# Kernel optimization log

Hardware: AMD Instinct MI355X
Metric: run time of the kernel (lower is better)

## Reference

```python
import jax, jax.numpy as jnp
import numpy as np

N_NODES = 60
N_EDGES = 1800
BATCH = 8192
NEG_SLOPE = 0.2  # PyG GATConv default leaky_relu slope


def _conv2d(x, w, b):
    y = jax.lax.conv_general_dilated(x, w, window_strides=(1, 1), padding='VALID',
                                     dimension_numbers=('NCHW', 'OIHW', 'NCHW'))
    return y + b[None, :, None, None]


def _maxpool2(x):
    return jax.lax.reduce_window(x, -jnp.inf, jax.lax.max, (1, 1, 2, 2), (1, 1, 2, 2), 'VALID')


def _gat(x, src, dst, edge_attr, W, a_src, a_dst, We, a_edge, b, n):
    # PyG GATConv, heads=1: xl = x W ; alpha_e = leakyrelu(a_src.xl[src] + a_dst.xl[dst] + a_edge.(edge_attr We))
    xl = x @ W                                    # [N, out]
    asrc = (xl * a_src).sum(-1)                   # [N]
    adst = (xl * a_dst).sum(-1)                   # [N]
    aedge = ((edge_attr @ We) * a_edge).sum(-1)   # [E]
    alpha = jax.nn.leaky_relu(asrc[src] + adst[dst] + aedge, NEG_SLOPE)
    # softmax over incoming edges of each dst node
    m = jax.ops.segment_max(alpha, dst, num_segments=n)
    ex = jnp.exp(alpha - m[dst])
    denom = jax.ops.segment_sum(ex, dst, num_segments=n)
    w_e = ex / denom[dst]
    out = jax.ops.segment_sum(w_e[:, None] * xl[src], dst, num_segments=n)
    return out + b


def _batchnorm_gnn(x):
    # torch code uses .item(): mean/std are detached python floats
    avg = jax.lax.stop_gradient(x.mean())
    std = jax.lax.stop_gradient(jnp.sqrt(((x - avg) ** 2).mean()))
    return (x - avg) / std


def setup_inputs() -> dict:
    key = jax.random.key(0)
    ks = jax.random.split(key, 24)
    f = lambda k, shape, scale=0.1: (jax.random.normal(k, shape, dtype=jnp.float32) * scale)
    inp = {
        'node_fea': jax.random.normal(ks[0], (N_NODES, 1), dtype=jnp.float32),
        'edge_fea': jax.random.normal(ks[1], (N_EDGES, 1), dtype=jnp.float32),
        'pic_fea': jax.random.normal(ks[2], (BATCH, 3, 32, 32), dtype=jnp.float32),
        'conv1_w': f(ks[3], (6, 3, 5, 5)), 'conv1_b': f(ks[4], (6,)),
        'conv2_w': f(ks[5], (16, 6, 5, 5)), 'conv2_b': f(ks[6], (16,)),
        'gat1_w': f(ks[7], (1, 6), 0.5), 'gat1_att_src': f(ks[8], (6,), 0.5),
        'gat1_att_dst': f(ks[9], (6,), 0.5), 'gat1_lin_edge': f(ks[10], (1, 6), 0.5),
        'gat1_att_edge': f(ks[11], (6,), 0.5), 'gat1_b': f(ks[12], (6,)),
        'gat2_w': f(ks[13], (6, 16), 0.3), 'gat2_att_src': f(ks[14], (16,), 0.3),
        'gat2_att_dst': f(ks[15], (16,), 0.3), 'gat2_lin_edge': f(ks[16], (1, 16), 0.3),
        'gat2_att_edge': f(ks[17], (16,), 0.3), 'gat2_b': f(ks[18], (16,)),
        'fc1_w': f(ks[19], (1360, 512), 0.03), 'fc1_b': f(ks[20], (512,)),
        'fc2_w': f(ks[21], (512, 10), 0.05), 'fc2_b': f(ks[22], (10,)),
        'edge_index': jax.random.randint(ks[23], (2, N_EDGES), 0, N_NODES, dtype=jnp.int64 if jax.config.jax_enable_x64 else jnp.int32),
    }
    return inp


def reference(node_fea, edge_fea, pic_fea,
              conv1_w, conv1_b, conv2_w, conv2_b,
              gat1_w, gat1_att_src, gat1_att_dst, gat1_lin_edge, gat1_att_edge, gat1_b,
              gat2_w, gat2_att_src, gat2_att_dst, gat2_lin_edge, gat2_att_edge, gat2_b,
              fc1_w, fc1_b, fc2_w, fc2_b, edge_index):
    n = node_fea.shape[0]
    # CNN branch: 32 -> 28 -> 14 -> 10 -> 5
    p = _maxpool2(jax.nn.relu(_conv2d(pic_fea, conv1_w, conv1_b)))
    p = _maxpool2(jax.nn.relu(_conv2d(p, conv2_w, conv2_b)))
    p = p.reshape(p.shape[0], -1)  # [B, 400]
    # add self loops (PyG default, fill_value='mean' for edge_attr)
    loop = jnp.arange(n)
    src = jnp.concatenate([edge_index[0], loop])
    dst = jnp.concatenate([edge_index[1], loop])
    ea = jnp.concatenate([edge_fea, jnp.broadcast_to(edge_fea.mean(0, keepdims=True), (n, edge_fea.shape[1]))], axis=0)
    # GNN branch
    x = _gat(node_fea, src, dst, ea, gat1_w, gat1_att_src, gat1_att_dst, gat1_lin_edge, gat1_att_edge, gat1_b, n)
    x = jax.nn.relu(_batchnorm_gnn(x))
    x = _gat(x, src, dst, ea, gat2_w, gat2_att_src, gat2_att_dst, gat2_lin_edge, gat2_att_edge, gat2_b, n)
    x = jax.nn.relu(_batchnorm_gnn(x))
    g = x.reshape(-1)  # [960]
    feat = jnp.concatenate([jnp.broadcast_to(g, (p.shape[0], g.shape[0])), p], axis=1)  # [B, 1360]
    h = jax.nn.relu(feat @ fc1_w + fc1_b)
    return jnp.tanh(h @ fc2_w + fc2_b)
```

## Files before the change

kernel.cpp:

```cpp
#include <hip/hip_runtime.h>
#include <math.h>

#define N_NODES 60
#define N_EDGES 1800
#define N_ETOT  1860
#define SLOPE   0.2f

#define SROW 36
#define SCH  (32 * SROW)
#define CROW 15
#define CCH  (14 * CROW)

struct ConvS {
    float simg[3 * SCH];
    float sw1[450];
    float sb1[8];
    float sw2[2400];
    float sb2[16];
    float c1[6 * CCH];
};
struct GnnS {
    float ea[N_ETOT];
    float alpha[N_ETOT];
    float x_in[960];
    float xl[960];
    float outb[960];
    float as_[N_NODES], ad_[N_NODES], den_[N_NODES];
    float red[256];
    unsigned char srcs[N_ETOT], dsts[N_ETOT];
    unsigned short csr[N_ETOT];
    int cnt[N_NODES], off[N_NODES + 4];
};
union SMem { ConvS c; GnnS g; };

__device__ __forceinline__ void block_reduce_sum(float v, float* red, float* out) {
    int tid = threadIdx.x;
    red[tid] = v;
    __syncthreads();
    for (int st = 128; st > 0; st >>= 1) {
        if (tid < st) red[tid] += red[tid + st];
        __syncthreads();
    }
    *out = red[0];
    __syncthreads();
}

__device__ void gat_layer(GnnS& S, const float* x_in, int in_dim, int out_dim,
                          const float* W, const float* a_src, const float* a_dst,
                          const float* We, const float* a_edge, const float* bias,
                          float* xl, float* outb) {
    const int tid = threadIdx.x, nt = blockDim.x;
    for (int idx = tid; idx < N_NODES * out_dim; idx += nt) {
        int i = idx / out_dim, j = idx % out_dim;
        float s = 0.f;
        for (int k = 0; k < in_dim; ++k) s += x_in[i * in_dim + k] * W[k * out_dim + j];
        xl[idx] = s;
    }
    __syncthreads();
    for (int i = tid; i < N_NODES; i += nt) {
        float s = 0.f, d = 0.f;
        for (int j = 0; j < out_dim; ++j) {
            s += xl[i * out_dim + j] * a_src[j];
            d += xl[i * out_dim + j] * a_dst[j];
        }
        S.as_[i] = s; S.ad_[i] = d;
    }
    float ecoef = 0.f;
    for (int j = 0; j < out_dim; ++j) ecoef += We[j] * a_edge[j];
    __syncthreads();
    for (int e = tid; e < N_ETOT; e += nt) {
        float a = S.as_[S.srcs[e]] + S.ad_[S.dsts[e]] + S.ea[e] * ecoef;
        S.alpha[e] = (a >= 0.f) ? a : SLOPE * a;
    }
    __syncthreads();
    for (int d = tid; d < N_NODES; d += nt) {
        float m = -INFINITY;
        for (int k = S.off[d]; k < S.off[d + 1]; ++k) m = fmaxf(m, S.alpha[S.csr[k]]);
        float den = 0.f;
        for (int k = S.off[d]; k < S.off[d + 1]; ++k) {
            int e = S.csr[k];
            float ex = expf(S.alpha[e] - m);
            S.alpha[e] = ex;
            den += ex;
        }
        S.den_[d] = den;
    }
    __syncthreads();
    for (int idx = tid; idx < N_NODES * out_dim; idx += nt) {
        int d = idx / out_dim, j = idx % out_dim;
        float s = 0.f;
        for (int k = S.off[d]; k < S.off[d + 1]; ++k) {
            int e = S.csr[k];
            s += S.alpha[e] * xl[(int)S.srcs[e] * out_dim + j];
        }
        outb[idx] = s / S.den_[d] + bias[j];
    }
    __syncthreads();
}

__device__ void bn_relu(GnnS& S, const float* v, float* dst, int n) {
    const int tid = threadIdx.x, nt = blockDim.x;
    float s = 0.f;
    for (int i = tid; i < n; i += nt) s += v[i];
    float tot;
    block_reduce_sum(s, S.red, &tot);
    float avg = tot / n;
    float s2 = 0.f;
    for (int i = tid; i < n; i += nt) { float d = v[i] - avg; s2 += d * d; }
    block_reduce_sum(s2, S.red, &tot);
    float stdv = sqrtf(tot / n);
    for (int i = tid; i < n; i += nt) dst[i] = fmaxf((v[i] - avg) / stdv, 0.f);
    __syncthreads();
}

__device__ void gnn_path(GnnS& S,
    const float* node_fea, const float* edge_fea, const int* eidx,
    const float* g1w, const float* g1as, const float* g1ad,
    const float* g1we, const float* g1ae, const float* g1b,
    const float* g2w, const float* g2as, const float* g2ad,
    const float* g2we, const float* g2ae, const float* g2b,
    const float* fc1w, const float* fc1b, float* gcontrib) {
    const int tid = threadIdx.x, nt = blockDim.x;
    float s = 0.f;
    for (int e = tid; e < N_EDGES; e += nt) s += edge_fea[e];
    float tot;
    block_reduce_sum(s, S.red, &tot);
    float emean = tot / N_EDGES;
    for (int e = tid; e < N_ETOT; e += nt) {
        if (e < N_EDGES) {
            S.ea[e] = edge_fea[e];
            S.srcs[e] = (unsigned char)eidx[e];
            S.dsts[e] = (unsigned char)eidx[N_EDGES + e];
        } else {
            S.ea[e] = emean;
            S.srcs[e] = (unsigned char)(e - N_EDGES);
            S.dsts[e] = (unsigned char)(e - N_EDGES);
        }
    }
    if (tid < N_NODES) S.x_in[tid] = node_fea[tid];
    __syncthreads();
    if (tid < N_NODES) {
        int c = 0;
        for (int e = 0; e < N_ETOT; ++e) c += (S.dsts[e] == tid);
        S.cnt[tid] = c;
    }
    __syncthreads();
    if (tid == 0) {
        S.off[0] = 0;
        for (int d = 0; d < N_NODES; ++d) S.off[d + 1] = S.off[d] + S.cnt[d];
    }
    __syncthreads();
    if (tid < N_NODES) {
        int k = S.off[tid];
        for (int e = 0; e < N_ETOT; ++e)
            if (S.dsts[e] == tid) S.csr[k++] = (unsigned short)e;
    }
    __syncthreads();

    gat_layer(S, S.x_in, 1, 6, g1w, g1as, g1ad, g1we, g1ae, g1b, S.xl, S.outb);
    bn_relu(S, S.outb, S.x_in, N_NODES * 6);
    gat_layer(S, S.x_in, 6, 16, g2w, g2as, g2ad, g2we, g2ae, g2b, S.xl, S.outb);
    bn_relu(S, S.outb, S.x_in, N_NODES * 16);

    for (int j = tid; j < 512; j += nt) {
        float acc = fc1b[j];
#pragma unroll 4
        for (int k = 0; k < 960; ++k) acc += S.x_in[k] * fc1w[(size_t)k * 512 + j];
        gcontrib[j] = acc;
    }
}

__device__ void conv_path(ConvS& C, int b,
                          const float* __restrict__ pic,
                          const float* __restrict__ w1, const float* __restrict__ b1,
                          const float* __restrict__ w2, const float* __restrict__ b2,
                          float* __restrict__ p) {
    const int tid = threadIdx.x;
    const float* img = pic + (size_t)b * 3072;
    for (int i = tid; i < 3072; i += 256) {
        int ic = i >> 10, rem = i & 1023, y = rem >> 5, x = rem & 31;
        C.simg[ic * SCH + y * SROW + x] = img[i];
    }
    for (int i = tid; i < 450; i += 256) C.sw1[i] = w1[i];
    if (tid < 6) C.sb1[tid] = b1[tid];
    for (int i = tid; i < 2400; i += 256) C.sw2[i] = w2[i];
    if (tid < 16) C.sb2[tid] = b2[tid];
    __syncthreads();

    for (int it = tid; it < 588; it += 256) {
        int oc = it / 98, r = it % 98, py = r / 7, q = r % 7;
        int y0 = 2 * py, x0 = 4 * q;
        float bias = C.sb1[oc];
        float acc[2][4];
#pragma unroll
        for (int dy = 0; dy < 2; ++dy)
#pragma unroll
            for (int xi = 0; xi < 4; ++xi) acc[dy][xi] = bias;
        for (int ic = 0; ic < 3; ++ic) {
            float wr[25];
            const float* wp = &C.sw1[oc * 75 + ic * 25];
#pragma unroll
            for (int t = 0; t < 25; ++t) wr[t] = wp[t];
            const int base = ic * SCH + y0 * SROW + x0;
#pragma unroll
            for (int i = 0; i < 6; ++i) {
                const float4* rp = (const float4*)&C.simg[base + i * SROW];
                float4 va = rp[0], vb = rp[1];
                float row[8] = {va.x, va.y, va.z, va.w, vb.x, vb.y, vb.z, vb.w};
#pragma unroll
                for (int dy = 0; dy < 2; ++dy) {
                    int ky = i - dy;
                    if (ky >= 0 && ky < 5) {
#pragma unroll
                        for (int xi = 0; xi < 4; ++xi) {
                            float s = 0.f;
#pragma unroll
                            for (int kx = 0; kx < 5; ++kx)
                                s += row[xi + kx] * wr[ky * 5 + kx];
                            acc[dy][xi] += s;
                        }
                    }
                }
            }
        }
#pragma unroll
        for (int sx = 0; sx < 2; ++sx) {
            float mx = fmaxf(fmaxf(acc[0][2 * sx], acc[0][2 * sx + 1]),
                             fmaxf(acc[1][2 * sx], acc[1][2 * sx + 1]));
            C.c1[oc * CCH + py * CROW + 2 * q + sx] = fmaxf(mx, 0.f);
        }
    }
    __syncthreads();

    if (tid < 240) {
        int oc = tid / 15, r = tid % 15, py = r / 3, g = r % 3;
        int y0 = 2 * py, x0 = 4 * g;
        float bias = C.sb2[oc];
        float acc[2][4];
#pragma unroll
        for (int dy = 0; dy < 2; ++dy)
#pragma unroll
            for (int xi = 0; xi < 4; ++xi) acc[dy][xi] = bias;
        for (int ic = 0; ic < 6; ++ic) {
            float wr[25];
            const float* wp = &C.sw2[oc * 150 + ic * 25];
#pragma unroll
            for (int t = 0; t < 25; ++t) wr[t] = wp[t];
            const int base = ic * CCH + y0 * CROW + x0;
#pragma unroll
            for (int i = 0; i < 6; ++i) {
                float row[8];
#pragma unroll
                for (int j = 0; j < 8; ++j) row[j] = C.c1[base + i * CROW + j];
#pragma unroll
                for (int dy = 0; dy < 2; ++dy) {
                    int ky = i - dy;
                    if (ky >= 0 && ky < 5) {
#pragma unroll
                        for (int xi = 0; xi < 4; ++xi) {
                            float s = 0.f;
#pragma unroll
                            for (int kx = 0; kx < 5; ++kx)
                                s += row[xi + kx] * wr[ky * 5 + kx];
                            acc[dy][xi] += s;
                        }
                    }
                }
            }
        }
        int nsx = (g < 2) ? 2 : 1;
        for (int sx = 0; sx < nsx; ++sx) {
            float mx = fmaxf(fmaxf(acc[0][2 * sx], acc[0][2 * sx + 1]),
                             fmaxf(acc[1][2 * sx], acc[1][2 * sx + 1]));
            p[(size_t)b * 400 + oc * 25 + py * 5 + 2 * g + sx] = fmaxf(mx, 0.f);
        }
    }
}

__global__ void __launch_bounds__(256, 4) fused_kernel(
    const float* __restrict__ node_fea, const float* __restrict__ edge_fea,
    const int* __restrict__ eidx,
    const float* g1w, const float* g1as, const float* g1ad,
    const float* g1we, const float* g1ae, const float* g1b,
    const float* g2w, const float* g2as, const float* g2ad,
    const float* g2we, const float* g2ae, const float* g2b,
    const float* __restrict__ fc1w, const float* __restrict__ fc1b,
    float* __restrict__ gcontrib,
    const float* __restrict__ pic,
    const float* __restrict__ c1w, const float* __restrict__ c1b,
    const float* __restrict__ c2w, const float* __restrict__ c2b,
    float* __restrict__ p) {
    __shared__ SMem u;
    if (blockIdx.x == 0) {
        gnn_path(u.g, node_fea, edge_fea, eidx,
                 g1w, g1as, g1ad, g1we, g1ae, g1b,
                 g2w, g2as, g2ad, g2we, g2ae, g2b,
                 fc1w, fc1b, gcontrib);
    } else {
        conv_path(u.c, blockIdx.x - 1, pic, c1w, c1b, c2w, c2b, p);
    }
}

#define FC1_ROWS 16
__global__ void __launch_bounds__(256) fc1_kernel(
    const float* __restrict__ p, const float* __restrict__ w,
    const float* __restrict__ gcontrib, float* __restrict__ h) {
    __shared__ float sp[FC1_ROWS * 400];
    const int tid = threadIdx.x;
    const size_t r0 = (size_t)blockIdx.x * FC1_ROWS;
    for (int i = tid; i < FC1_ROWS * 400; i += 256) sp[i] = p[r0 * 400 + i];
    __syncthreads();
    const int c0 = tid, c1 = tid + 256;
    float acc[FC1_ROWS][2];
#pragma unroll
    for (int r = 0; r < FC1_ROWS; ++r) { acc[r][0] = 0.f; acc[r][1] = 0.f; }
    for (int k = 0; k < 400; k += 4) {
        float wa0 = w[(size_t)(k + 0) * 512 + c0], wa1 = w[(size_t)(k + 0) * 512 + c1];
        float wb0 = w[(size_t)(k + 1) * 512 + c0], wb1 = w[(size_t)(k + 1) * 512 + c1];
        float wc0 = w[(size_t)(k + 2) * 512 + c0], wc1 = w[(size_t)(k + 2) * 512 + c1];
        float wd0 = w[(size_t)(k + 3) * 512 + c0], wd1 = w[(size_t)(k + 3) * 512 + c1];
#pragma unroll
        for (int r = 0; r < FC1_ROWS; ++r) {
            float4 pv = *(const float4*)&sp[r * 400 + k];
            acc[r][0] += pv.x * wa0 + pv.y * wb0 + pv.z * wc0 + pv.w * wd0;
            acc[r][1] += pv.x * wa1 + pv.y * wb1 + pv.z * wc1 + pv.w * wd1;
        }
    }
    float g0 = gcontrib[c0], g1 = gcontrib[c1];
#pragma unroll
    for (int r = 0; r < FC1_ROWS; ++r) {
        h[(r0 + r) * 512 + c0] = fmaxf(acc[r][0] + g0, 0.f);
        h[(r0 + r) * 512 + c1] = fmaxf(acc[r][1] + g1, 0.f);
    }
}

__global__ void __launch_bounds__(256) fc2_kernel(
    const float* __restrict__ h, const float* __restrict__ w,
    const float* __restrict__ b, float* __restrict__ out) {
    const int wave = threadIdx.x >> 6, lane = threadIdx.x & 63;
    const size_t row = (size_t)blockIdx.x * 4 + wave;
    const float* hr = h + row * 512;
    float partial[10];
#pragma unroll
    for (int j = 0; j < 10; ++j) partial[j] = 0.f;
    for (int k = lane; k < 512; k += 64) {
        float hv = hr[k];
        const float* wr = w + (size_t)k * 10;
#pragma unroll
        for (int j = 0; j < 10; ++j) partial[j] += hv * wr[j];
    }
#pragma unroll
    for (int j = 0; j < 10; ++j) {
        float v = partial[j];
        for (int sft = 32; sft > 0; sft >>= 1) v += __shfl_xor(v, sft, 64);
        partial[j] = v;
    }
    if (lane == 0) {
#pragma unroll
        for (int j = 0; j < 10; ++j)
            out[row * 10 + j] = tanhf(partial[j] + b[j]);
    }
}

extern "C" void kernel_launch(void* const* d_in, const int* in_sizes, int n_in,
                              void* d_out, int out_size, void* d_ws, size_t ws_size,
                              hipStream_t stream) {
    const float* node_fea = (const float*)d_in[0];
    const float* edge_fea = (const float*)d_in[1];
    const float* pic      = (const float*)d_in[2];
    const float* c1w = (const float*)d_in[3];
    const float* c1b = (const float*)d_in[4];
    const float* c2w = (const float*)d_in[5];
    const float* c2b = (const float*)d_in[6];
    const float* g1w  = (const float*)d_in[7];
    const float* g1as = (const float*)d_in[8];
    const float* g1ad = (const float*)d_in[9];
    const float* g1we = (const float*)d_in[10];
    const float* g1ae = (const float*)d_in[11];
    const float* g1b  = (const float*)d_in[12];
    const float* g2w  = (const float*)d_in[13];
    const float* g2as = (const float*)d_in[14];
    const float* g2ad = (const float*)d_in[15];
    const float* g2we = (const float*)d_in[16];
    const float* g2ae = (const float*)d_in[17];
    const float* g2b  = (const float*)d_in[18];
    const float* fc1w = (const float*)d_in[19];
    const float* fc1b = (const float*)d_in[20];
    const float* fc2w = (const float*)d_in[21];
    const float* fc2b = (const float*)d_in[22];
    const int*   eidx = (const int*)d_in[23];
    float* out = (float*)d_out;

    char* ws = (char*)d_ws;
    float* gcontrib = (float*)ws;
    float* p = (float*)(ws + 2048);
    float* h = (float*)(ws + 2048 + (size_t)8192 * 400 * 4);

    hipLaunchKernelGGL(fused_kernel, dim3(8193), dim3(256), 0, stream,
                       node_fea, edge_fea, eidx,
                       g1w, g1as, g1ad, g1we, g1ae, g1b,
                       g2w, g2as, g2ad, g2we, g2ae, g2b,
                       fc1w, fc1b, gcontrib,
                       pic, c1w, c1b, c2w, c2b, p);
    hipLaunchKernelGGL(fc1_kernel, dim3(8192 / FC1_ROWS), dim3(256), 0, stream,
                       p, fc1w + (size_t)960 * 512, gcontrib, h);
    hipLaunchKernelGGL(fc2_kernel, dim3(8192 / 4), dim3(256), 0, stream,
                       h, fc2w, fc2b, out);
}
```

Measured before the change: 490.7 us.

## Retune conv shared-memory layout, thread mapping and occupancy; slim GNN smem

```diff
diff --git a/kernel.cpp b/kernel.cpp
--- a/kernel.cpp
+++ b/kernel.cpp
@@ -6,25 +6,21 @@
 #define N_ETOT  1860
 #define SLOPE   0.2f
 
-#define SROW 36
+#define SROW 34
 #define SCH  (32 * SROW)
-#define CROW 15
+#define CROW 16
 #define CCH  (14 * CROW)
-
 struct ConvS {
     float simg[3 * SCH];
-    float sw1[450];
-    float sb1[8];
-    float sw2[2400];
-    float sb2[16];
+    float sw1[456], sb1[8];
+    float sw2[2400], sb2[16];
     float c1[6 * CCH];
+    float pad[8];
 };
 struct GnnS {
-    float ea[N_ETOT];
     float alpha[N_ETOT];
     float x_in[960];
     float xl[960];
-    float outb[960];
     float as_[N_NODES], ad_[N_NODES], den_[N_NODES];
     float red[256];
     unsigned char srcs[N_ETOT], dsts[N_ETOT];
@@ -48,6 +44,7 @@
 __device__ void gat_layer(GnnS& S, const float* x_in, int in_dim, int out_dim,
                           const float* W, const float* a_src, const float* a_dst,
                           const float* We, const float* a_edge, const float* bias,
+                          const float* edge_fea, float emean,
                           float* xl, float* outb) {
     const int tid = threadIdx.x, nt = blockDim.x;
     for (int idx = tid; idx < N_NODES * out_dim; idx += nt) {
@@ -69,7 +66,8 @@
     for (int j = 0; j < out_dim; ++j) ecoef += We[j] * a_edge[j];
     __syncthreads();
     for (int e = tid; e < N_ETOT; e += nt) {
-        float a = S.as_[S.srcs[e]] + S.ad_[S.dsts[e]] + S.ea[e] * ecoef;
+        float eaval = (e < N_EDGES) ? edge_fea[e] : emean;
+        float a = S.as_[S.srcs[e]] + S.ad_[S.dsts[e]] + eaval * ecoef;
         S.alpha[e] = (a >= 0.f) ? a : SLOPE * a;
     }
     __syncthreads();
@@ -98,7 +96,7 @@
     __syncthreads();
 }
 
-__device__ void bn_relu(GnnS& S, const float* v, float* dst, int n) {
+__device__ void bn_relu(GnnS& S, float* v, int n) {
     const int tid = threadIdx.x, nt = blockDim.x;
     float s = 0.f;
     for (int i = tid; i < n; i += nt) s += v[i];
@@ -109,7 +107,8 @@
     for (int i = tid; i < n; i += nt) { float d = v[i] - avg; s2 += d * d; }
     block_reduce_sum(s2, S.red, &tot);
     float stdv = sqrtf(tot / n);
-    for (int i = tid; i < n; i += nt) dst[i] = fmaxf((v[i] - avg) / stdv, 0.f);
+    __syncthreads();
+    for (int i = tid; i < n; i += nt) v[i] = fmaxf((v[i] - avg) / stdv, 0.f);
     __syncthreads();
 }
 
@@ -128,11 +127,9 @@
     float emean = tot / N_EDGES;
     for (int e = tid; e < N_ETOT; e += nt) {
         if (e < N_EDGES) {
-            S.ea[e] = edge_fea[e];
             S.srcs[e] = (unsigned char)eidx[e];
             S.dsts[e] = (unsigned char)eidx[N_EDGES + e];
         } else {
-            S.ea[e] = emean;
             S.srcs[e] = (unsigned char)(e - N_EDGES);
             S.dsts[e] = (unsigned char)(e - N_EDGES);
         }
@@ -157,10 +154,12 @@
     }
     __syncthreads();
 
-    gat_layer(S, S.x_in, 1, 6, g1w, g1as, g1ad, g1we, g1ae, g1b, S.xl, S.outb);
-    bn_relu(S, S.outb, S.x_in, N_NODES * 6);
-    gat_layer(S, S.x_in, 6, 16, g2w, g2as, g2ad, g2we, g2ae, g2b, S.xl, S.outb);
-    bn_relu(S, S.outb, S.x_in, N_NODES * 16);
+    gat_layer(S, S.x_in, 1, 6, g1w, g1as, g1ad, g1we, g1ae, g1b,
+              edge_fea, emean, S.xl, S.x_in);
+    bn_relu(S, S.x_in, N_NODES * 6);
+    gat_layer(S, S.x_in, 6, 16, g2w, g2as, g2ad, g2we, g2ae, g2b,
+              edge_fea, emean, S.xl, S.x_in);
+    bn_relu(S, S.x_in, N_NODES * 16);
 
     for (int j = tid; j < 512; j += nt) {
         float acc = fc1b[j];
@@ -170,16 +169,19 @@
     }
 }
 
-__device__ void conv_path(ConvS& C, int b,
+__device__ void conv_path(ConvS& C, int img,
                           const float* __restrict__ pic,
                           const float* __restrict__ w1, const float* __restrict__ b1,
                           const float* __restrict__ w2, const float* __restrict__ b2,
                           float* __restrict__ p) {
     const int tid = threadIdx.x;
-    const float* img = pic + (size_t)b * 3072;
-    for (int i = tid; i < 3072; i += 256) {
-        int ic = i >> 10, rem = i & 1023, y = rem >> 5, x = rem & 31;
-        C.simg[ic * SCH + y * SROW + x] = img[i];
+
+    for (int i = tid; i < 768; i += 256) {
+        float4 v = ((const float4*)(pic + (size_t)img * 3072))[i];
+        int e = 4 * i, ic = e >> 10, rem = e & 1023, y = rem >> 5, x = rem & 31;
+        float2* dst = (float2*)&C.simg[ic * SCH + y * SROW + x];
+        dst[0] = make_float2(v.x, v.y);
+        dst[1] = make_float2(v.z, v.w);
     }
     for (int i = tid; i < 450; i += 256) C.sw1[i] = w1[i];
     if (tid < 6) C.sb1[tid] = b1[tid];
@@ -188,36 +190,37 @@
     __syncthreads();
 
     for (int it = tid; it < 588; it += 256) {
-        int oc = it / 98, r = it % 98, py = r / 7, q = r % 7;
-        int y0 = 2 * py, x0 = 4 * q;
+        int py = it / 42, r = it % 42, oc = r / 7, qx = r % 7;
+        int y0 = 2 * py, x0 = 4 * qx;
         float bias = C.sb1[oc];
         float acc[2][4];
 #pragma unroll
         for (int dy = 0; dy < 2; ++dy)
 #pragma unroll
-            for (int xi = 0; xi < 4; ++xi) acc[dy][xi] = bias;
+            for (int dx = 0; dx < 4; ++dx) acc[dy][dx] = bias;
+
+#pragma unroll 1
         for (int ic = 0; ic < 3; ++ic) {
             float wr[25];
-            const float* wp = &C.sw1[oc * 75 + ic * 25];
-#pragma unroll
-            for (int t = 0; t < 25; ++t) wr[t] = wp[t];
-            const int base = ic * SCH + y0 * SROW + x0;
+#pragma unroll
+            for (int k = 0; k < 25; ++k) wr[k] = C.sw1[oc * 75 + ic * 25 + k];
+            const float* B = &C.simg[ic * SCH + y0 * SROW + x0];
 #pragma unroll
             for (int i = 0; i < 6; ++i) {
-                const float4* rp = (const float4*)&C.simg[base + i * SROW];
-                float4 va = rp[0], vb = rp[1];
-                float row[8] = {va.x, va.y, va.z, va.w, vb.x, vb.y, vb.z, vb.w};
+                const float2* rp = (const float2*)(B + i * SROW);
+                float2 A = rp[0], Bv = rp[1], Cv = rp[2], Dv = rp[3];
+                float row[8] = {A.x, A.y, Bv.x, Bv.y, Cv.x, Cv.y, Dv.x, Dv.y};
 #pragma unroll
                 for (int dy = 0; dy < 2; ++dy) {
                     int ky = i - dy;
                     if (ky >= 0 && ky < 5) {
 #pragma unroll
-                        for (int xi = 0; xi < 4; ++xi) {
+                        for (int dx = 0; dx < 4; ++dx) {
                             float s = 0.f;
 #pragma unroll
                             for (int kx = 0; kx < 5; ++kx)
-                                s += row[xi + kx] * wr[ky * 5 + kx];
-                            acc[dy][xi] += s;
+                                s += row[dx + kx] * wr[ky * 5 + kx];
+                            acc[dy][dx] += s;
                         }
                     }
                 }
@@ -225,59 +228,59 @@
         }
 #pragma unroll
         for (int sx = 0; sx < 2; ++sx) {
-            float mx = fmaxf(fmaxf(acc[0][2 * sx], acc[0][2 * sx + 1]),
-                             fmaxf(acc[1][2 * sx], acc[1][2 * sx + 1]));
-            C.c1[oc * CCH + py * CROW + 2 * q + sx] = fmaxf(mx, 0.f);
+            float m = fmaxf(fmaxf(acc[0][2 * sx], acc[0][2 * sx + 1]),
+                            fmaxf(acc[1][2 * sx], acc[1][2 * sx + 1]));
+            C.c1[oc * CCH + py * CROW + 2 * qx + sx] = fmaxf(m, 0.f);
         }
     }
     __syncthreads();
 
     if (tid < 240) {
-        int oc = tid / 15, r = tid % 15, py = r / 3, g = r % 3;
+        int py = tid / 48, r = tid % 48, oc = r / 3, g = r % 3;
         int y0 = 2 * py, x0 = 4 * g;
         float bias = C.sb2[oc];
         float acc[2][4];
 #pragma unroll
         for (int dy = 0; dy < 2; ++dy)
 #pragma unroll
-            for (int xi = 0; xi < 4; ++xi) acc[dy][xi] = bias;
+            for (int dx = 0; dx < 4; ++dx) acc[dy][dx] = bias;
+
+#pragma unroll 1
         for (int ic = 0; ic < 6; ++ic) {
             float wr[25];
-            const float* wp = &C.sw2[oc * 150 + ic * 25];
-#pragma unroll
-            for (int t = 0; t < 25; ++t) wr[t] = wp[t];
-            const int base = ic * CCH + y0 * CROW + x0;
+#pragma unroll
+            for (int k = 0; k < 25; ++k) wr[k] = C.sw2[oc * 150 + ic * 25 + k];
+            const float* B = &C.c1[ic * CCH + y0 * CROW + x0];
 #pragma unroll
             for (int i = 0; i < 6; ++i) {
-                float row[8];
-#pragma unroll
-                for (int j = 0; j < 8; ++j) row[j] = C.c1[base + i * CROW + j];
+                const float2* rp = (const float2*)(B + i * CROW);
+                float2 A = rp[0], Bv = rp[1], Cv = rp[2], Dv = rp[3];
+                float row[8] = {A.x, A.y, Bv.x, Bv.y, Cv.x, Cv.y, Dv.x, Dv.y};
 #pragma unroll
                 for (int dy = 0; dy < 2; ++dy) {
                     int ky = i - dy;
                     if (ky >= 0 && ky < 5) {
 #pragma unroll
-                        for (int xi = 0; xi < 4; ++xi) {
+                        for (int dx = 0; dx < 4; ++dx) {
                             float s = 0.f;
 #pragma unroll
                             for (int kx = 0; kx < 5; ++kx)
-                                s += row[xi + kx] * wr[ky * 5 + kx];
-                            acc[dy][xi] += s;
+                                s += row[dx + kx] * wr[ky * 5 + kx];
+                            acc[dy][dx] += s;
                         }
                     }
                 }
             }
         }
-        int nsx = (g < 2) ? 2 : 1;
-        for (int sx = 0; sx < nsx; ++sx) {
-            float mx = fmaxf(fmaxf(acc[0][2 * sx], acc[0][2 * sx + 1]),
-                             fmaxf(acc[1][2 * sx], acc[1][2 * sx + 1]));
-            p[(size_t)b * 400 + oc * 25 + py * 5 + 2 * g + sx] = fmaxf(mx, 0.f);
-        }
-    }
-}
-
-__global__ void __launch_bounds__(256, 4) fused_kernel(
+        float m0 = fmaxf(fmaxf(acc[0][0], acc[0][1]), fmaxf(acc[1][0], acc[1][1]));
+        float m1 = fmaxf(fmaxf(acc[0][2], acc[0][3]), fmaxf(acc[1][2], acc[1][3]));
+        float* prow = p + ((size_t)img * 16 + oc) * 25 + py * 5;
+        prow[2 * g] = fmaxf(m0, 0.f);
+        if (g < 2) prow[2 * g + 1] = fmaxf(m1, 0.f);
+    }
+}
+
+__global__ void __launch_bounds__(256, 5) fused_kernel(
     const float* __restrict__ node_fea, const float* __restrict__ edge_fea,
     const int* __restrict__ eidx,
     const float* g1w, const float* g1as, const float* g1ad,
@@ -302,7 +305,7 @@
 }
 
 #define FC1_ROWS 16
-__global__ void __launch_bounds__(256) fc1_kernel(
+__global__ void fc1_kernel(
     const float* __restrict__ p, const float* __restrict__ w,
     const float* __restrict__ gcontrib, float* __restrict__ h) {
     __shared__ float sp[FC1_ROWS * 400];
@@ -334,7 +337,7 @@
     }
 }
 
-__global__ void __launch_bounds__(256) fc2_kernel(
+__global__ void fc2_kernel(
     const float* __restrict__ h, const float* __restrict__ w,
     const float* __restrict__ b, float* __restrict__ out) {
     const int wave = threadIdx.x >> 6, lane = threadIdx.x & 63;
```

New measurement: 456.3 us. -7.0%, faster.
